# Performance work log

Measured on AMD Instinct MI355X. Metric: run time of the kernel, lower is better.

Reference implementation:

```python
import jax, jax.numpy as jnp
import numpy as np

TEMPERATURE = 0.07
N, D, NUM_CLASSES = 8192, 1024, 128


def setup_inputs() -> dict:
    key = jax.random.key(0)
    k1, k2 = jax.random.split(key)
    embeddings = jax.random.normal(k1, (N, D), dtype=jnp.float32)
    labels = jax.random.randint(k2, (N,), 0, NUM_CLASSES, dtype=jnp.int64)
    return {"embeddings": embeddings, "labels": labels}


def reference(embeddings, labels):
    # L2-normalize rows (eps matches F.normalize default clamp of 1e-12 on the norm)
    norm = jnp.maximum(jnp.linalg.norm(embeddings, axis=-1, keepdims=True), 1e-12)
    emb = embeddings / norm
    # [N, N] similarity scaled by temperature
    sim = jnp.matmul(emb, emb.T) / TEMPERATURE
    # positive mask: same label, diagonal zeroed
    pos_mask = (labels[:, None] == labels[None, :]).astype(sim.dtype)
    pos_mask = pos_mask * (1.0 - jnp.eye(sim.shape[0], dtype=sim.dtype))
    exp_sim = jnp.exp(sim)
    sum_exp = exp_sim.sum(axis=1)              # [N]
    pos_sum = (exp_sim * pos_mask).sum(axis=1)  # [N]
    loss = -jnp.log(pos_sum / sum_exp)
    return loss.mean()
```

## Files before the change

### kernel.cpp

```cpp
#include <hip/hip_runtime.h>
#include <hip/hip_bf16.h>
#include <math.h>

#define N 8192
#define D 1024
#define BM 256
#define BK 32
#define NTIL 32
#define NBLK 528
#define KSTEPS 32
#define BUFSZ 16384

typedef __bf16 bf16_t;
typedef bf16_t bf16x4 __attribute__((ext_vector_type(4)));
typedef bf16_t bf16x8 __attribute__((ext_vector_type(8)));
typedef float f32x4 __attribute__((ext_vector_type(4)));

__global__ __launch_bounds__(256) void norm_cast(const float* __restrict__ in,
                                                 bf16_t* __restrict__ out,
                                                 float* __restrict__ sumExp,
                                                 float* __restrict__ posSum) {
    const int wave = threadIdx.x >> 6, lane = threadIdx.x & 63;
    const int row  = blockIdx.x * 4 + wave;
    const float4* src = (const float4*)(in + (size_t)row * D);
    float4 v[4];
    float ss = 0.f;
    #pragma unroll
    for (int i = 0; i < 4; ++i) {
        v[i] = src[lane + 64 * i];
        ss += v[i].x * v[i].x + v[i].y * v[i].y + v[i].z * v[i].z + v[i].w * v[i].w;
    }
    #pragma unroll
    for (int off = 32; off >= 1; off >>= 1) ss += __shfl_xor(ss, off, 64);
    const float scale = 1.0f / fmaxf(sqrtf(ss), 1e-12f);
    bf16x4* dst = (bf16x4*)(out + (size_t)row * D);
    #pragma unroll
    for (int i = 0; i < 4; ++i) {
        bf16x4 o;
        o[0] = (bf16_t)(v[i].x * scale);
        o[1] = (bf16_t)(v[i].y * scale);
        o[2] = (bf16_t)(v[i].z * scale);
        o[3] = (bf16_t)(v[i].w * scale);
        dst[lane + 64 * i] = o;
    }
    if (lane == 0) { sumExp[row] = 0.f; posSum[row] = 0.f; }
}

__global__ __launch_bounds__(512, 2) void gemm_fused(const bf16_t* __restrict__ E,
                                                     const int* __restrict__ labels,
                                                     float* __restrict__ sumExp,
                                                     float* __restrict__ posSum) {
    __shared__ bf16_t As[4][256 * 32];
    __shared__ bf16_t Bs[4][256 * 32];

    const int b0 = blockIdx.x;
    const int b  = (b0 & 7) * (NBLK / 8) + (b0 >> 3);

    int ti = (int)((sqrtf(8.0f * (float)b + 1.0f) - 1.0f) * 0.5f);
    while ((ti + 1) * (ti + 2) / 2 <= b) ++ti;
    while (ti * (ti + 1) / 2 > b) --ti;
    const int tj = b - ti * (ti + 1) / 2;
    const bool isDiag = (ti == tj);

    const int tid  = threadIdx.x;
    const int wave = tid >> 6;
    const int lane = tid & 63;
    const int lr   = lane & 15;
    const int q    = lane >> 4;
    const int wm   = wave >> 2;
    const int wn   = wave & 3;
    const int rowStart = ti * BM;
    const int colStart = tj * BM;

    f32x4 acc[8][4];
    #pragma unroll
    for (int m = 0; m < 8; ++m)
        #pragma unroll
        for (int n = 0; n < 4; ++n) acc[m][n] = {0.f, 0.f, 0.f, 0.f};

    const int r0  = tid >> 2;
    const int lu0 = (tid & 3) ^ (r0 & 3);
    const char* gA = (const char*)(E + (size_t)rowStart * D) + (size_t)r0 * (D * 2) + lu0 * 16;
    const char* gB = (const char*)(E + (size_t)colStart * D) + (size_t)r0 * (D * 2) + lu0 * 16;

    #define STAGE_A2(bi, kb) do {                                                        \
        const char* g_ = gA + (kb);                                                      \
        char* l_ = (char*)&As[bi][0] + wave * 1024;                                      \
        __builtin_amdgcn_global_load_lds((const __attribute__((address_space(1))) void*)g_, \
            (__attribute__((address_space(3))) void*)l_, 16, 0, 0);                      \
        __builtin_amdgcn_global_load_lds(                                                \
            (const __attribute__((address_space(1))) void*)(g_ + 128 * 2048),            \
            (__attribute__((address_space(3))) void*)(l_ + 8192), 16, 0, 0);             \
    } while (0)
    #define STAGE_B2(bi, kb) do {                                                        \
        const char* g_ = gB + (kb);                                                      \
        char* l_ = (char*)&Bs[bi][0] + wave * 1024;                                      \
        __builtin_amdgcn_global_load_lds((const __attribute__((address_space(1))) void*)g_, \
            (__attribute__((address_space(3))) void*)l_, 16, 0, 0);                      \
        __builtin_amdgcn_global_load_lds(                                                \
            (const __attribute__((address_space(1))) void*)(g_ + 128 * 2048),            \
            (__attribute__((address_space(3))) void*)(l_ + 8192), 16, 0, 0);             \
    } while (0)

    const int su = (q ^ (lr & 3)) * 16;

    #define LD4(DST, RBASE, OFFB) do {                                                   \
        _Pragma("unroll")                                                                \
        for (int i_ = 0; i_ < 4; ++i_)                                                   \
            DST[i_] = *(const bf16x8*)((RBASE) + (OFFB) + i_ * 1024 + su);               \
    } while (0)
    #define MFMA16(AF, BF, MO) do {                                                      \
        _Pragma("unroll")                                                                \
        for (int m_ = 0; m_ < 4; ++m_) {                                                 \
            _Pragma("unroll")                                                            \
            for (int n_ = 0; n_ < 4; ++n_)                                               \
                acc[(MO) + m_][n_] = __builtin_amdgcn_mfma_f32_16x16x32_bf16(            \
                    AF[m_], BF[n_], acc[(MO) + m_][n_], 0, 0, 0);                        \
        }                                                                                \
    } while (0)
    #define PHASE_MID() do {                                                             \
        __builtin_amdgcn_s_barrier();                                                    \
        asm volatile("s_waitcnt lgkmcnt(0)");                                            \
        __builtin_amdgcn_sched_barrier(0);                                               \
        __builtin_amdgcn_s_setprio(1);                                                   \
    } while (0)
    #define PHASE_END() do {                                                             \
        __builtin_amdgcn_s_setprio(0);                                                   \
        __builtin_amdgcn_s_barrier();                                                    \
    } while (0)

    bf16x8 af[4], bfr[4];

    STAGE_A2(0, 0);   STAGE_B2(0, 0);
    STAGE_A2(1, 64);  STAGE_B2(1, 64);
    STAGE_A2(2, 128); STAGE_B2(2, 128);
    asm volatile("s_waitcnt vmcnt(8)" ::: "memory");
    __builtin_amdgcn_sched_barrier(0);
    __builtin_amdgcn_s_barrier();

    #pragma unroll 1
    for (int s = 0; s < KSTEPS; ++s) {
        const int bi   = s & 3;
        const int bnxt = (s + 3) & 3;
        const int kb   = (s + 3) * 64;
        const bool doStage = (s <= KSTEPS - 4);
        const char* aBase = (const char*)&As[bi][0] + (wm * 128 + lr) * 64;
        const char* bBase = (const char*)&Bs[bi][0] + (wn * 64 + lr) * 64;

        LD4(af,  aBase, 0);
        LD4(bfr, bBase, 0);
        if (doStage) STAGE_A2(bnxt, kb);
        PHASE_MID();
        MFMA16(af, bfr, 0);
        PHASE_END();

        LD4(af, aBase, 4096);
        if (doStage) STAGE_B2(bnxt, kb);
        if (s <= KSTEPS - 4)      asm volatile("s_waitcnt vmcnt(8)" ::: "memory");
        else if (s == KSTEPS - 3) asm volatile("s_waitcnt vmcnt(4)" ::: "memory");
        else                      asm volatile("s_waitcnt vmcnt(0)" ::: "memory");
        __builtin_amdgcn_sched_barrier(0);
        PHASE_MID();
        MFMA16(af, bfr, 4);
        PHASE_END();
    }

    const float invT = 1.0f / 0.07f;
    int lc[4];
    #pragma unroll
    for (int n = 0; n < 4; ++n)
        lc[n] = labels[colStart + wn * 64 + n * 16 + lr];

    float colAll[4] = {0.f, 0.f, 0.f, 0.f};
    float colPos[4] = {0.f, 0.f, 0.f, 0.f};
    #pragma unroll
    for (int m = 0; m < 8; ++m) {
        #pragma unroll
        for (int e = 0; e < 4; ++e) {
            const int rloc = wm * 128 + m * 16 + q * 4 + e;
            const int gi   = rowStart + rloc;
            const int li   = labels[gi];
            float s_all = 0.f, s_pos = 0.f;
            #pragma unroll
            for (int n = 0; n < 4; ++n) {
                const int cloc = wn * 64 + n * 16 + lr;
                const int gj   = colStart + cloc;
                const float v  = __expf(acc[m][n][e] * invT);
                const bool same = (lc[n] == li);
                s_all += v;
                if (same && gi != gj) s_pos += v;
                if (!isDiag) {
                    colAll[n] += v;
                    if (same) colPos[n] += v;
                }
            }
            #pragma unroll
            for (int off = 1; off < 16; off <<= 1) {
                s_all += __shfl_xor(s_all, off, 64);
                s_pos += __shfl_xor(s_pos, off, 64);
            }
            if (lr == 0) {
                atomicAdd(&sumExp[gi], s_all);
                atomicAdd(&posSum[gi], s_pos);
            }
        }
    }
    if (!isDiag) {
        #pragma unroll
        for (int n = 0; n < 4; ++n) {
            float a = colAll[n], p = colPos[n];
            a += __shfl_xor(a, 16, 64);  a += __shfl_xor(a, 32, 64);
            p += __shfl_xor(p, 16, 64);  p += __shfl_xor(p, 32, 64);
            if (q == 0) {
                const int gj = colStart + wn * 64 + n * 16 + lr;
                atomicAdd(&sumExp[gj], a);
                atomicAdd(&posSum[gj], p);
            }
        }
    }
}

__global__ __launch_bounds__(1024) void finalize(const float* __restrict__ sumExp,
                                                 const float* __restrict__ posSum,
                                                 float* __restrict__ out) {
    const int tid = threadIdx.x;
    float s = 0.f;
    #pragma unroll
    for (int i = tid; i < N; i += 1024)
        s += __logf(sumExp[i] / posSum[i]);
    #pragma unroll
    for (int off = 32; off >= 1; off >>= 1) s += __shfl_xor(s, off, 64);
    __shared__ float red[16];
    if ((tid & 63) == 0) red[tid >> 6] = s;
    __syncthreads();
    if (tid == 0) {
        float t = 0.f;
        #pragma unroll
        for (int i = 0; i < 16; ++i) t += red[i];
        out[0] = t / (float)N;
    }
}

extern "C" void kernel_launch(void* const* d_in, const int* in_sizes, int n_in,
                              void* d_out, int out_size, void* d_ws, size_t ws_size,
                              hipStream_t stream) {
    const float* emb    = (const float*)d_in[0];
    const int*   labels = (const int*)d_in[1];
    float* out = (float*)d_out;

    float*  sumExp = (float*)d_ws;
    float*  posSum = sumExp + N;
    bf16_t* EN     = (bf16_t*)((char*)d_ws + (size_t)2 * N * sizeof(float));

    norm_cast<<<N / 4, 256, 0, stream>>>(emb, EN, sumExp, posSum);

    gemm_fused<<<NBLK, 512, 0, stream>>>(EN, labels, sumExp, posSum);

    finalize<<<1, 1024, 0, stream>>>(sumExp, posSum, out);
}
```

Measured before the change: 229.1 us.

## Halve column tile to 128 and use three-stage LDS pipeline with more blocks

Changes the fused GEMM tile from 256x256 to 256x128, which doubles the number of triangular blocks. Block-index decoding is reworked for half-width column tiles, and both halves of a diagonal tile are treated as diagonal. The LDS ring buffer drops from four stages to three, staging is merged into one macro, and launch bounds now request four blocks per CU. The aim is better load balance and occupancy. In exchange, each block reuses its data less and B traffic per FLOP goes up, and the LDS footprint may still cap how many blocks fit on a CU.

```diff
diff --git a/kernel.cpp b/kernel.cpp
--- a/kernel.cpp
+++ b/kernel.cpp
@@ -5,11 +5,10 @@
 #define N 8192
 #define D 1024
 #define BM 256
+#define BN 128
 #define BK 32
-#define NTIL 32
-#define NBLK 528
+#define NBLK 1056
 #define KSTEPS 32
-#define BUFSZ 16384
 
 typedef __bf16 bf16_t;
 typedef bf16_t bf16x4 __attribute__((ext_vector_type(4)));
@@ -46,21 +45,21 @@
     if (lane == 0) { sumExp[row] = 0.f; posSum[row] = 0.f; }
 }
 
-__global__ __launch_bounds__(512, 2) void gemm_fused(const bf16_t* __restrict__ E,
+__global__ __launch_bounds__(512, 4) void gemm_fused(const bf16_t* __restrict__ E,
                                                      const int* __restrict__ labels,
                                                      float* __restrict__ sumExp,
                                                      float* __restrict__ posSum) {
-    __shared__ bf16_t As[4][256 * 32];
-    __shared__ bf16_t Bs[4][256 * 32];
+    __shared__ bf16_t As[3][256 * 32];
+    __shared__ bf16_t Bs[3][128 * 32];
 
     const int b0 = blockIdx.x;
     const int b  = (b0 & 7) * (NBLK / 8) + (b0 >> 3);
 
-    int ti = (int)((sqrtf(8.0f * (float)b + 1.0f) - 1.0f) * 0.5f);
-    while ((ti + 1) * (ti + 2) / 2 <= b) ++ti;
-    while (ti * (ti + 1) / 2 > b) --ti;
-    const int tj = b - ti * (ti + 1) / 2;
-    const bool isDiag = (ti == tj);
+    int ti = (int)((sqrtf(4.0f * (float)b + 1.0f) - 1.0f) * 0.5f);
+    while ((ti + 1) * (ti + 2) <= b) ++ti;
+    while (ti * (ti + 1) > b) --ti;
+    const int tj2 = b - ti * (ti + 1);
+    const bool isDiag = ((tj2 >> 1) == ti);
 
     const int tid  = threadIdx.x;
     const int wave = tid >> 6;
@@ -70,52 +69,43 @@
     const int wm   = wave >> 2;
     const int wn   = wave & 3;
     const int rowStart = ti * BM;
-    const int colStart = tj * BM;
-
-    f32x4 acc[8][4];
-    #pragma unroll
-    for (int m = 0; m < 8; ++m)
-        #pragma unroll
-        for (int n = 0; n < 4; ++n) acc[m][n] = {0.f, 0.f, 0.f, 0.f};
+    const int colStart = tj2 * BN;
+
+    f32x4 acc[8][2];
+    #pragma unroll
+    for (int m = 0; m < 8; ++m) {
+        acc[m][0] = {0.f, 0.f, 0.f, 0.f};
+        acc[m][1] = {0.f, 0.f, 0.f, 0.f};
+    }
 
     const int r0  = tid >> 2;
-    const int lu0 = (tid & 3) ^ (r0 & 3);
+    const int lu0 = (tid & 3) ^ ((r0 >> 1) & 3);
     const char* gA = (const char*)(E + (size_t)rowStart * D) + (size_t)r0 * (D * 2) + lu0 * 16;
     const char* gB = (const char*)(E + (size_t)colStart * D) + (size_t)r0 * (D * 2) + lu0 * 16;
 
-    #define STAGE_A2(bi, kb) do {                                                        \
-        const char* g_ = gA + (kb);                                                      \
-        char* l_ = (char*)&As[bi][0] + wave * 1024;                                      \
-        __builtin_amdgcn_global_load_lds((const __attribute__((address_space(1))) void*)g_, \
-            (__attribute__((address_space(3))) void*)l_, 16, 0, 0);                      \
+    #define STAGE_T(T, BI) do {                                                          \
+        const char* ga_ = gA + (size_t)(T) * 64;                                         \
+        const char* gb_ = gB + (size_t)(T) * 64;                                         \
+        char* la_ = (char*)&As[BI][0] + wave * 1024;                                     \
+        char* lb_ = (char*)&Bs[BI][0] + wave * 1024;                                     \
+        __builtin_amdgcn_global_load_lds((const __attribute__((address_space(1))) void*)ga_, \
+            (__attribute__((address_space(3))) void*)la_, 16, 0, 0);                     \
         __builtin_amdgcn_global_load_lds(                                                \
-            (const __attribute__((address_space(1))) void*)(g_ + 128 * 2048),            \
-            (__attribute__((address_space(3))) void*)(l_ + 8192), 16, 0, 0);             \
-    } while (0)
-    #define STAGE_B2(bi, kb) do {                                                        \
-        const char* g_ = gB + (kb);                                                      \
-        char* l_ = (char*)&Bs[bi][0] + wave * 1024;                                      \
-        __builtin_amdgcn_global_load_lds((const __attribute__((address_space(1))) void*)g_, \
-            (__attribute__((address_space(3))) void*)l_, 16, 0, 0);                      \
-        __builtin_amdgcn_global_load_lds(                                                \
-            (const __attribute__((address_space(1))) void*)(g_ + 128 * 2048),            \
-            (__attribute__((address_space(3))) void*)(l_ + 8192), 16, 0, 0);             \
-    } while (0)
-
-    const int su = (q ^ (lr & 3)) * 16;
-
-    #define LD4(DST, RBASE, OFFB) do {                                                   \
-        _Pragma("unroll")                                                                \
-        for (int i_ = 0; i_ < 4; ++i_)                                                   \
-            DST[i_] = *(const bf16x8*)((RBASE) + (OFFB) + i_ * 1024 + su);               \
-    } while (0)
-    #define MFMA16(AF, BF, MO) do {                                                      \
+            (const __attribute__((address_space(1))) void*)(ga_ + 128 * 2048),           \
+            (__attribute__((address_space(3))) void*)(la_ + 8192), 16, 0, 0);            \
+        __builtin_amdgcn_global_load_lds((const __attribute__((address_space(1))) void*)gb_, \
+            (__attribute__((address_space(3))) void*)lb_, 16, 0, 0);                     \
+    } while (0)
+
+    const int su = (q ^ ((lr >> 1) & 3)) * 16;
+
+    #define MFMA8(MO) do {                                                               \
         _Pragma("unroll")                                                                \
         for (int m_ = 0; m_ < 4; ++m_) {                                                 \
             _Pragma("unroll")                                                            \
-            for (int n_ = 0; n_ < 4; ++n_)                                               \
+            for (int n_ = 0; n_ < 2; ++n_)                                               \
                 acc[(MO) + m_][n_] = __builtin_amdgcn_mfma_f32_16x16x32_bf16(            \
-                    AF[m_], BF[n_], acc[(MO) + m_][n_], 0, 0, 0);                        \
+                    af[m_], bfr[n_], acc[(MO) + m_][n_], 0, 0, 0);                       \
         }                                                                                \
     } while (0)
     #define PHASE_MID() do {                                                             \
@@ -129,50 +119,52 @@
         __builtin_amdgcn_s_barrier();                                                    \
     } while (0)
 
-    bf16x8 af[4], bfr[4];
-
-    STAGE_A2(0, 0);   STAGE_B2(0, 0);
-    STAGE_A2(1, 64);  STAGE_B2(1, 64);
-    STAGE_A2(2, 128); STAGE_B2(2, 128);
-    asm volatile("s_waitcnt vmcnt(8)" ::: "memory");
+    #define STEP(T, BI, BI2, DOSTAGE, VMASM) do {                                        \
+        const char* aB_ = (const char*)&As[BI][0] + (wm * 128 + lr) * 64 + su;           \
+        const char* bB_ = (const char*)&Bs[BI][0] + (wn * 32 + lr) * 64 + su;            \
+        _Pragma("unroll")                                                                \
+        for (int m_ = 0; m_ < 4; ++m_)                                                   \
+            af[m_] = *(const bf16x8*)(aB_ + m_ * 1024);                                  \
+        bfr[0] = *(const bf16x8*)(bB_);                                                  \
+        bfr[1] = *(const bf16x8*)(bB_ + 1024);                                           \
+        if (DOSTAGE) STAGE_T((T) + 2, BI2);                                              \
+        PHASE_MID();                                                                     \
+        MFMA8(0);                                                                        \
+        PHASE_END();                                                                     \
+        _Pragma("unroll")                                                                \
+        for (int m_ = 0; m_ < 4; ++m_)                                                   \
+            af[m_] = *(const bf16x8*)(aB_ + (4 + m_) * 1024);                            \
+        asm volatile(VMASM ::: "memory");                                                \
+        __builtin_amdgcn_sched_barrier(0);                                               \
+        PHASE_MID();                                                                     \
+        MFMA8(4);                                                                        \
+        PHASE_END();                                                                     \
+    } while (0)
+
+    bf16x8 af[4], bfr[2];
+
+    STAGE_T(0, 0);
+    STAGE_T(1, 1);
+    asm volatile("s_waitcnt vmcnt(3)" ::: "memory");
     __builtin_amdgcn_sched_barrier(0);
     __builtin_amdgcn_s_barrier();
 
     #pragma unroll 1
-    for (int s = 0; s < KSTEPS; ++s) {
-        const int bi   = s & 3;
-        const int bnxt = (s + 3) & 3;
-        const int kb   = (s + 3) * 64;
-        const bool doStage = (s <= KSTEPS - 4);
-        const char* aBase = (const char*)&As[bi][0] + (wm * 128 + lr) * 64;
-        const char* bBase = (const char*)&Bs[bi][0] + (wn * 64 + lr) * 64;
-
-        LD4(af,  aBase, 0);
-        LD4(bfr, bBase, 0);
-        if (doStage) STAGE_A2(bnxt, kb);
-        PHASE_MID();
-        MFMA16(af, bfr, 0);
-        PHASE_END();
-
-        LD4(af, aBase, 4096);
-        if (doStage) STAGE_B2(bnxt, kb);
-        if (s <= KSTEPS - 4)      asm volatile("s_waitcnt vmcnt(8)" ::: "memory");
-        else if (s == KSTEPS - 3) asm volatile("s_waitcnt vmcnt(4)" ::: "memory");
-        else                      asm volatile("s_waitcnt vmcnt(0)" ::: "memory");
-        __builtin_amdgcn_sched_barrier(0);
-        PHASE_MID();
-        MFMA16(af, bfr, 4);
-        PHASE_END();
-    }
+    for (int tt = 0; tt < 30; tt += 3) {
+        STEP(tt,     0, 2, true, "s_waitcnt vmcnt(3)");
+        STEP(tt + 1, 1, 0, true, "s_waitcnt vmcnt(3)");
+        STEP(tt + 2, 2, 1, true, "s_waitcnt vmcnt(3)");
+    }
+    STEP(30, 0, 2, false, "s_waitcnt vmcnt(0)");
+    STEP(31, 1, 0, false, "s_waitcnt vmcnt(0)");
 
     const float invT = 1.0f / 0.07f;
-    int lc[4];
-    #pragma unroll
-    for (int n = 0; n < 4; ++n)
-        lc[n] = labels[colStart + wn * 64 + n * 16 + lr];
-
-    float colAll[4] = {0.f, 0.f, 0.f, 0.f};
-    float colPos[4] = {0.f, 0.f, 0.f, 0.f};
+    int lc[2];
+    lc[0] = labels[colStart + wn * 32 + lr];
+    lc[1] = labels[colStart + wn * 32 + 16 + lr];
+
+    float colAll[2] = {0.f, 0.f};
+    float colPos[2] = {0.f, 0.f};
     #pragma unroll
     for (int m = 0; m < 8; ++m) {
         #pragma unroll
@@ -182,8 +174,8 @@
             const int li   = labels[gi];
             float s_all = 0.f, s_pos = 0.f;
             #pragma unroll
-            for (int n = 0; n < 4; ++n) {
-                const int cloc = wn * 64 + n * 16 + lr;
+            for (int n = 0; n < 2; ++n) {
+                const int cloc = wn * 32 + n * 16 + lr;
                 const int gj   = colStart + cloc;
                 const float v  = __expf(acc[m][n][e] * invT);
                 const bool same = (lc[n] == li);
@@ -207,12 +199,12 @@
     }
     if (!isDiag) {
         #pragma unroll
-        for (int n = 0; n < 4; ++n) {
+        for (int n = 0; n < 2; ++n) {
             float a = colAll[n], p = colPos[n];
             a += __shfl_xor(a, 16, 64);  a += __shfl_xor(a, 32, 64);
             p += __shfl_xor(p, 16, 64);  p += __shfl_xor(p, 32, 64);
             if (q == 0) {
-                const int gj = colStart + wn * 64 + n * 16 + lr;
+                const int gj = colStart + wn * 32 + n * 16 + lr;
                 atomicAdd(&sumExp[gj], a);
                 atomicAdd(&posSum[gj], p);
             }
```

Result: no change. 230.3 us (+0.5%).
